# Kernel tuning notes

Hardware: AMD Instinct MI355X
Metric: run time of the kernel (lower is better)

The kernel has to match this reference:

```python
import jax, jax.numpy as jnp
import numpy as np

D_MODEL = 2048
STATE = 16
KCONV = 4
EXPAND = 2
D_INNER = D_MODEL * EXPAND
EPS = 1e-05


def setup_inputs() -> dict:
    key = jax.random.key(0)
    ks = jax.random.split(key, 10)
    s = 0.02
    x = jax.random.normal(ks[0], (2, 2048, D_MODEL), dtype=jnp.float32)
    norm_w = jnp.ones((D_MODEL,), jnp.float32)
    in_proj_w = jax.random.normal(ks[1], (D_INNER * 2, D_MODEL), jnp.float32) * s
    conv_w = jax.random.normal(ks[2], (D_INNER, 1, KCONV), jnp.float32) * s  # depthwise (O,I/g,K)
    conv_b = jnp.zeros((D_INNER,), jnp.float32)
    x_proj_w = jax.random.normal(ks[3], (STATE * 2 + 1, D_INNER), jnp.float32) * s
    dt_w = jax.random.normal(ks[4], (D_INNER, 1), jnp.float32) * s
    dt_b = jnp.zeros((D_INNER,), jnp.float32)
    A_log = jnp.log(jnp.broadcast_to(jnp.arange(1, STATE + 1, dtype=jnp.float32)[None, :], (D_INNER, STATE)))
    D_param = jnp.ones((D_INNER,), jnp.float32)
    out_proj_w = jax.random.normal(ks[5], (D_MODEL, D_INNER), jnp.float32) * s
    return {"x": x, "norm_w": norm_w, "in_proj_w": in_proj_w, "conv_w": conv_w,
            "conv_b": conv_b, "x_proj_w": x_proj_w, "dt_w": dt_w, "dt_b": dt_b,
            "A_log": A_log, "D_param": D_param, "out_proj_w": out_proj_w}


def _silu(v):
    return v * jax.nn.sigmoid(v)


def reference(x, norm_w, in_proj_w, conv_w, conv_b, x_proj_w, dt_w, dt_b, A_log, D_param, out_proj_w):
    residual = x
    # RMSNorm
    xn = x * jax.lax.rsqrt(jnp.mean(x * x, axis=-1, keepdims=True) + EPS) * norm_w
    # in_proj -> split into x_inner, z
    xz = jnp.einsum('bld,ed->ble', xn, in_proj_w)  # [B,L,2*d_inner]
    x_inner, z = jnp.split(xz, 2, axis=-1)
    # causal depthwise conv1d (torch pads K-1 both sides then truncates to L == left pad only)
    xc = jnp.transpose(x_inner, (0, 2, 1))  # [B,d_inner,L]
    xc = jax.lax.conv_general_dilated(
        xc, conv_w, window_strides=(1,), padding=[(KCONV - 1, 0)],
        dimension_numbers=('NCH', 'OIH', 'NCH'), feature_group_count=D_INNER)
    xc = xc + conv_b[None, :, None]
    xc = _silu(jnp.transpose(xc, (0, 2, 1)))  # [B,L,d_inner]
    # SSM parameter projections
    x_ssm = jnp.einsum('bld,ed->ble', xc, x_proj_w)  # [B,L,2N+1]
    dt = jax.nn.softplus(x_ssm[..., -1:] * dt_w[:, 0] + dt_b)  # [B,L,d_inner]
    B_p = x_ssm[..., :STATE]            # [B,L,N]
    C_p = x_ssm[..., STATE:2 * STATE]   # [B,L,N]
    A = -jnp.exp(A_log)                 # [d_inner,N]

    batch = x.shape[0]
    h0 = jnp.zeros((batch, D_INNER, STATE), x.dtype)

    def step(h, inp):
        dt_t, B_t, C_t, u_t = inp  # [B,d_inner],[B,N],[B,N],[B,d_inner]
        dA = jnp.exp(dt_t[..., None] * A)  # [B,d_inner,N]
        h = dA * h + (dt_t * u_t)[..., None] * B_t[:, None, :]
        y_t = jnp.sum(h * C_t[:, None, :], axis=-1) + D_param * u_t
        return h, y_t

    seq_first = lambda a: jnp.swapaxes(a, 0, 1)
    _, ys = jax.lax.scan(step, h0, (seq_first(dt), seq_first(B_p), seq_first(C_p), seq_first(xc)))
    y = jnp.swapaxes(ys, 0, 1)  # [B,L,d_inner]
    y = y * _silu(z)
    return jnp.einsum('ble,de->bld', y, out_proj_w) + residual
```

## Files before the change

### kernel.cpp

```cpp
#include <hip/hip_runtime.h>

#define NTOK   4096
#define LSEQ   2048
#define DMODEL 2048
#define DINNER 4096
#define NSTATE 16
#define NCHAIN 8192

using short8 = __attribute__((ext_vector_type(8))) short;
using f32x4  = __attribute__((ext_vector_type(4))) float;

__device__ inline float b2f(short s) {
    union { unsigned u; float f; } v;
    v.u = ((unsigned)(unsigned short)s) << 16;
    return v.f;
}
__device__ inline short f2b(float f) {
    unsigned u = __float_as_uint(f);
    unsigned r = (u + 0x7fffu + ((u >> 16) & 1u)) >> 16;
    return (short)r;
}

template <int OFF>
__device__ inline float swz(float v) {
    return __int_as_float(__builtin_amdgcn_ds_swizzle(__float_as_int(v), OFF));
}
template <int CTRL>
__device__ inline float qperm(float v) {
    return __int_as_float(
        __builtin_amdgcn_mov_dpp(__float_as_int(v), CTRL, 0xF, 0xF, true));
}

__global__ __launch_bounds__(256) void f32_to_bf16_kernel(
    const float* __restrict__ in, short* __restrict__ out, int n8) {
    int i = blockIdx.x * 256 + threadIdx.x;
    if (i >= n8) return;
    const float4* p = (const float4*)in + 2 * (size_t)i;
    float4 a = p[0], b = p[1];
    short8 s;
    s[0] = f2b(a.x); s[1] = f2b(a.y); s[2] = f2b(a.z); s[3] = f2b(a.w);
    s[4] = f2b(b.x); s[5] = f2b(b.y); s[6] = f2b(b.z); s[7] = f2b(b.w);
    *(short8*)(out + 8 * (size_t)i) = s;
}

__global__ __launch_bounds__(256) void rmsnorm_kernel(
    const float* __restrict__ x, const float* __restrict__ w,
    short* __restrict__ xn) {
    const int t = blockIdx.x, tid = threadIdx.x;
    const float4* xr = (const float4*)(x + (size_t)t * DMODEL + tid * 8);
    float4 a = xr[0], b = xr[1];
    float v[8] = {a.x, a.y, a.z, a.w, b.x, b.y, b.z, b.w};
    float ss = 0.f;
#pragma unroll
    for (int j = 0; j < 8; ++j) ss += v[j] * v[j];
#pragma unroll
    for (int o = 32; o > 0; o >>= 1) ss += __shfl_down(ss, o, 64);
    __shared__ float sred[4];
    if ((tid & 63) == 0) sred[tid >> 6] = ss;
    __syncthreads();
    float r = rsqrtf((sred[0] + sred[1] + sred[2] + sred[3]) * (1.f / DMODEL) + 1e-5f);
    const float4* wr = (const float4*)(w + tid * 8);
    float4 wa = wr[0], wb = wr[1];
    float wv[8] = {wa.x, wa.y, wa.z, wa.w, wb.x, wb.y, wb.z, wb.w};
    short8 o8;
#pragma unroll
    for (int j = 0; j < 8; ++j) o8[j] = f2b(v[j] * r * wv[j]);
    *(short8*)(xn + (size_t)t * DMODEL + tid * 8) = o8;
}

template <bool ADD_RES, bool F32OUT, bool SPLIT>
__global__ __launch_bounds__(256) void gemm_bt(
    const short* __restrict__ A, const short* __restrict__ B,
    const float* __restrict__ RES, void* __restrict__ Cp, void* __restrict__ Cp2,
    int M, int N, int K) {
    __shared__ __align__(16) short As[128 * 32];
    __shared__ __align__(16) short Bs[128 * 32];

    const int tid  = threadIdx.x;
    const int wave = tid >> 6;
    const int lane = tid & 63;
    const int lr   = lane & 15;
    const int q    = lane >> 4;
    const int m0   = blockIdx.x * 128;
    const int n0   = blockIdx.y * 128;
    const int wm   = (wave >> 1) * 64;
    const int wn   = (wave & 1) * 64;

    f32x4 acc[4][4] = {};

    for (int k0 = 0; k0 < K; k0 += 32) {
#pragma unroll
        for (int p = 0; p < 2; ++p) {
            int i16 = p * 256 + tid;
            int row = i16 >> 2, ch = i16 & 3;
            const short* ga = A + (size_t)(m0 + row) * K + k0 + ch * 8;
            const short* gb = B + (size_t)(n0 + row) * K + k0 + ch * 8;
            __builtin_amdgcn_global_load_lds(
                (const __attribute__((address_space(1))) void*)ga,
                (__attribute__((address_space(3))) void*)((char*)As + i16 * 16),
                16, 0, 0);
            __builtin_amdgcn_global_load_lds(
                (const __attribute__((address_space(1))) void*)gb,
                (__attribute__((address_space(3))) void*)((char*)Bs + i16 * 16),
                16, 0, 0);
        }
        __syncthreads();

        short8 af[4], bfr[4];
#pragma unroll
        for (int i = 0; i < 4; ++i) {
            af[i]  = *(const short8*)&As[(wm + i * 16 + lr) * 32 + q * 8];
            bfr[i] = *(const short8*)&Bs[(wn + i * 16 + lr) * 32 + q * 8];
        }
#pragma unroll
        for (int i = 0; i < 4; ++i)
#pragma unroll
            for (int j = 0; j < 4; ++j)
                acc[i][j] = __builtin_amdgcn_mfma_f32_16x16x32_bf16(
                    af[i], bfr[j], acc[i][j], 0, 0, 0);
        __syncthreads();
    }

    short* sdst = nullptr;
    int    noff = 0;
    if (SPLIT) {
        bool hi = (n0 >= DINNER);
        sdst = hi ? (short*)Cp2 : (short*)Cp;
        noff = hi ? DINNER : 0;
    }

#pragma unroll
    for (int i = 0; i < 4; ++i)
#pragma unroll
        for (int j = 0; j < 4; ++j)
#pragma unroll
            for (int r = 0; r < 4; ++r) {
                int m = m0 + wm + i * 16 + q * 4 + r;
                int n = n0 + wn + j * 16 + lr;
                float v = acc[i][j][r];
                if (SPLIT) {
                    sdst[(size_t)m * DINNER + (n - noff)] = f2b(v);
                } else {
                    size_t idx = (size_t)m * N + n;
                    if (ADD_RES) v += RES[idx];
                    if (F32OUT) ((float*)Cp)[idx] = v;
                    else        ((short*)Cp)[idx] = f2b(v);
                }
            }
}

__global__ __launch_bounds__(256) void conv_silu_t_kernel(
    const short* __restrict__ xi, const float* __restrict__ cw,
    const float* __restrict__ cb, short* __restrict__ xc,
    short* __restrict__ uT) {
    __shared__ short tin[67][72];
    __shared__ short tout[64][72];
    const int bb = blockIdx.z;
    const int l0 = blockIdx.x * 64;
    const int c0 = blockIdx.y * 64;
    const int tid = threadIdx.x;

    for (int idx = tid; idx < 67 * 8; idx += 256) {
        int row = idx >> 3, cs = (idx & 7) * 8;
        int ls = l0 - 3 + row;
        short8 v;
        if (ls >= 0) {
            v = *(const short8*)(xi + ((size_t)(bb * LSEQ + ls)) * DINNER + c0 + cs);
        } else {
#pragma unroll
            for (int j = 0; j < 8; ++j) v[j] = 0;
        }
        *(short8*)&tin[row][cs] = v;
    }
    __syncthreads();

    const int r   = tid >> 2;
    const int cb16 = (tid & 3) * 16;
    short8 a[4][2];
#pragma unroll
    for (int k = 0; k < 4; ++k) {
        a[k][0] = *(const short8*)&tin[r + k][cb16];
        a[k][1] = *(const short8*)&tin[r + k][cb16 + 8];
    }
    short o16[16];
#pragma unroll
    for (int j = 0; j < 16; ++j) {
        const int c = c0 + cb16 + j;
        float4 w4 = *(const float4*)(cw + (size_t)c * 4);
        float acc = cb[c];
        acc += b2f(a[0][j >> 3][j & 7]) * w4.x;
        acc += b2f(a[1][j >> 3][j & 7]) * w4.y;
        acc += b2f(a[2][j >> 3][j & 7]) * w4.z;
        acc += b2f(a[3][j >> 3][j & 7]) * w4.w;
        o16[j] = f2b(acc / (1.f + __expf(-acc)));
    }
    {
        short8 lo, hi;
#pragma unroll
        for (int j = 0; j < 8; ++j) { lo[j] = o16[j]; hi[j] = o16[8 + j]; }
        short* dst = xc + ((size_t)(bb * LSEQ + l0 + r)) * DINNER + c0 + cb16;
        *(short8*)dst = lo;
        *(short8*)(dst + 8) = hi;
    }
#pragma unroll
    for (int j = 0; j < 16; ++j) tout[r][cb16 + j] = o16[j];
    __syncthreads();

    const int rr = tid >> 3;
    const int l8 = (tid & 7) * 8;
#pragma unroll
    for (int p = 0; p < 2; ++p) {
        int cr = p * 32 + rr;
        short8 v;
#pragma unroll
        for (int j = 0; j < 8; ++j) v[j] = tout[l8 + j][cr];
        *(short8*)(uT + ((size_t)(bb * DINNER + c0 + cr)) * LSEQ + l0 + l8) = v;
    }
}

__global__ __launch_bounds__(256) void xproj_kernel(
    const short* __restrict__ xc, const float* __restrict__ W,
    float* __restrict__ BT, float* __restrict__ CT, float* __restrict__ s32T) {
    const int t0 = blockIdx.x * 2, tid = threadIdx.x;
    float xv0[16], xv1[16];
    {
        short8 a = *(const short8*)(xc + (size_t)t0 * DINNER + tid * 16);
        short8 b = *(const short8*)(xc + (size_t)t0 * DINNER + tid * 16 + 8);
        short8 c = *(const short8*)(xc + (size_t)(t0 + 1) * DINNER + tid * 16);
        short8 d = *(const short8*)(xc + (size_t)(t0 + 1) * DINNER + tid * 16 + 8);
#pragma unroll
        for (int j = 0; j < 8; ++j) {
            xv0[j] = b2f(a[j]); xv0[8 + j] = b2f(b[j]);
            xv1[j] = b2f(c[j]); xv1[8 + j] = b2f(d[j]);
        }
    }
    float acc0[33], acc1[33];
#pragma unroll
    for (int e = 0; e < 33; ++e) {
        const float4* wr = (const float4*)(W + (size_t)e * DINNER + tid * 16);
        float4 w0 = wr[0], w1 = wr[1], w2 = wr[2], w3 = wr[3];
        float wv[16] = {w0.x, w0.y, w0.z, w0.w, w1.x, w1.y, w1.z, w1.w,
                        w2.x, w2.y, w2.z, w2.w, w3.x, w3.y, w3.z, w3.w};
        float s0 = 0.f, s1 = 0.f;
#pragma unroll
        for (int j = 0; j < 16; ++j) { s0 += xv0[j] * wv[j]; s1 += xv1[j] * wv[j]; }
        acc0[e] = s0; acc1[e] = s1;
    }
    __shared__ float red[4][33];
#pragma unroll
    for (int tk = 0; tk < 2; ++tk) {
#pragma unroll
        for (int e = 0; e < 33; ++e) {
            float v = tk ? acc1[e] : acc0[e];
#pragma unroll
            for (int o = 32; o > 0; o >>= 1) v += __shfl_down(v, o, 64);
            if ((tid & 63) == 0) red[tid >> 6][e] = v;
        }
        __syncthreads();
        if (tid < 33) {
            float val = red[0][tid] + red[1][tid] + red[2][tid] + red[3][tid];
            const int t = t0 + tk;
            const int bb = t >> 11, l = t & (LSEQ - 1);
            if (tid < 16)
                BT[((size_t)bb * NSTATE + tid) * LSEQ + l] = val;
            else if (tid < 32)
                CT[((size_t)bb * NSTATE + (tid - 16)) * LSEQ + l] = val;
            else
                s32T[(size_t)bb * LSEQ + l] = val;
        }
        __syncthreads();
    }
}

__global__ __launch_bounds__(256) void dt_kernel(
    const float* __restrict__ s32T, const float* __restrict__ dt_w,
    const float* __restrict__ dt_b, float* __restrict__ dtT0,
    float* __restrict__ dtT1) {
    const int chain = blockIdx.x;
    const int b = chain >> 12;
    const int c = chain & (DINNER - 1);
    const float dtw = dt_w[c], dtb = dt_b[c];
    const float* src = s32T + (size_t)b * LSEQ + threadIdx.x * 8;
    float* dst = (b ? dtT1 : dtT0) + (size_t)c * LSEQ + threadIdx.x * 8;
    float4 s0 = ((const float4*)src)[0], s1 = ((const float4*)src)[1];
    float sv[8] = {s0.x, s0.y, s0.z, s0.w, s1.x, s1.y, s1.z, s1.w};
    float dv[8];
#pragma unroll
    for (int j = 0; j < 8; ++j) {
        float v = sv[j] * dtw + dtb;
        dv[j] = (v > 20.f) ? v : __logf(1.f + __expf(v));
    }
    ((float4*)dst)[0] = make_float4(dv[0], dv[1], dv[2], dv[3]);
    ((float4*)dst)[1] = make_float4(dv[4], dv[5], dv[6], dv[7]);
}

#define GQ 4
__global__ __launch_bounds__(256) void scan_state_kernel(
    const float* __restrict__ BT, const float* __restrict__ CT,
    const float* __restrict__ dtT0, const float* __restrict__ dtT1,
    const short* __restrict__ uT, const short* __restrict__ Z,
    short* __restrict__ yout,
    const float* __restrict__ A_log, const float* __restrict__ D_par) {
    const int tid   = threadIdx.x;
    const int n     = tid & 15;
    const int chain = blockIdx.x * 16 + (tid >> 4);
    const int b     = chain >> 12;
    const int c     = chain & (DINNER - 1);

    const float An = -__expf(A_log[c * NSTATE + n]);
    const float Dp = D_par[c];

    const float* Bb = BT + ((size_t)b * NSTATE + n) * LSEQ;
    const float* Cb = CT + ((size_t)b * NSTATE + n) * LSEQ;
    const float* db = (b ? dtT1 : dtT0) + (size_t)c * LSEQ;
    const short* ub = uT + (size_t)chain * LSEQ;
    const short* ue = ub + n;
    const short* zp = Z + ((size_t)b * LSEQ + n) * DINNER + c;
    short*       yp = yout + ((size_t)b * LSEQ + n) * DINNER + c;

    f32x4 Bq[GQ], Cq[GQ], dq[GQ];
    uint2 uq[GQ];
#pragma unroll
    for (int g = 0; g < GQ; ++g) {
        Bq[g] = *(const f32x4*)(Bb + g * 4);
        Cq[g] = *(const f32x4*)(Cb + g * 4);
        dq[g] = *(const f32x4*)(db + g * 4);
        uq[g] = *(const uint2*)(ub + g * 4);
    }

    float h = 0.f;
    for (int l0 = 0; l0 < LSEQ; l0 += 16) {
        const float u_n = b2f(ue[0]);
        const float z_n = b2f(zp[0]);
        float ys = 0.f;
#pragma unroll
        for (int g = 0; g < GQ; ++g) {
            f32x4 B4 = Bq[g], C4 = Cq[g], d4 = dq[g];
            uint2 u4 = uq[g];
            int lp  = l0 + 16 + g * 4;
            int lpc = (lp > LSEQ - 4) ? (LSEQ - 4) : lp;
            Bq[g] = *(const f32x4*)(Bb + lpc);
            Cq[g] = *(const f32x4*)(Cb + lpc);
            dq[g] = *(const f32x4*)(db + lpc);
            uq[g] = *(const uint2*)(ub + lpc);

            float uv[4], e[4];
#pragma unroll
            for (int i = 0; i < 4; ++i) {
                unsigned uw = (i < 2) ? u4.x : u4.y;
                union { unsigned uu; float ff; } t;
                t.uu = (i & 1) ? (uw & 0xffff0000u) : (uw << 16);
                uv[i] = t.ff;
                e[i]  = __expf(d4[i] * An);
            }
            float part[4];
#pragma unroll
            for (int i = 0; i < 4; ++i) {
                h = e[i] * h + (d4[i] * uv[i]) * B4[i];
                part[i] = h * C4[i];
            }
            float tmp[4];
#pragma unroll
            for (int i = 0; i < 4; ++i) tmp[i] = swz<0x201F>(part[i]);
#pragma unroll
            for (int i = 0; i < 4; ++i) part[i] += tmp[i];
#pragma unroll
            for (int i = 0; i < 4; ++i) tmp[i] = swz<0x101F>(part[i]);
#pragma unroll
            for (int i = 0; i < 4; ++i) part[i] += tmp[i];
#pragma unroll
            for (int i = 0; i < 4; ++i) part[i] += qperm<0x4E>(part[i]);
#pragma unroll
            for (int i = 0; i < 4; ++i) part[i] += qperm<0xB1>(part[i]);
#pragma unroll
            for (int i = 0; i < 4; ++i) ys = (n == g * 4 + i) ? part[i] : ys;
        }
        float y  = ys + Dp * u_n;
        float zg = z_n / (1.f + __expf(-z_n));
        yp[0] = f2b(y * zg);
        ue += 16;
        zp += (size_t)16 * DINNER;
        yp += (size_t)16 * DINNER;
    }
}

extern "C" void kernel_launch(void* const* d_in, const int* in_sizes, int n_in,
                              void* d_out, int out_size, void* d_ws, size_t ws_size,
                              hipStream_t stream) {
    const float* x      = (const float*)d_in[0];
    const float* norm_w = (const float*)d_in[1];
    const float* w_in   = (const float*)d_in[2];
    const float* conv_w = (const float*)d_in[3];
    const float* conv_b = (const float*)d_in[4];
    const float* w_xp   = (const float*)d_in[5];
    const float* dt_w   = (const float*)d_in[6];
    const float* dt_b   = (const float*)d_in[7];
    const float* A_log  = (const float*)d_in[8];
    const float* D_par  = (const float*)d_in[9];
    const float* w_out  = (const float*)d_in[10];
    float* out = (float*)d_out;

    char* ws = (char*)d_ws;
    short* wb   = (short*)(ws);
    short* xn   = (short*)(ws + (size_t)(32 << 20));
    short* Xi   = (short*)(ws + (size_t)(48 << 20));
    short* Zb   = (short*)(ws + (size_t)(80 << 20));
    short* xc   = (short*)(ws + (size_t)(112 << 20));
    float* BT   = (float*)(ws + (size_t)(144 << 20));
    float* CT   = (float*)(ws + (size_t)(144 << 20) + (256 << 10));
    float* s32T = (float*)(ws + (size_t)(144 << 20) + (512 << 10));
    float* dtT0 = (float*)Xi;
    float* dtT1 = out;

    f32_to_bf16_kernel<<<(2 * DINNER * DMODEL / 8) / 256, 256, 0, stream>>>(
        w_in, wb, 2 * DINNER * DMODEL / 8);
    rmsnorm_kernel<<<NTOK, 256, 0, stream>>>(x, norm_w, xn);
    gemm_bt<false, false, true><<<dim3(NTOK / 128, 8192 / 128), 256, 0, stream>>>(
        xn, wb, nullptr, Xi, Zb, NTOK, 2 * DINNER, DMODEL);
    conv_silu_t_kernel<<<dim3(LSEQ / 64, DINNER / 64, 2), 256, 0, stream>>>(
        Xi, conv_w, conv_b, xc, wb);
    xproj_kernel<<<NTOK / 2, 256, 0, stream>>>(xc, w_xp, BT, CT, s32T);
    dt_kernel<<<NCHAIN, 256, 0, stream>>>(s32T, dt_w, dt_b, dtT0, dtT1);
    scan_state_kernel<<<NCHAIN / 16, 256, 0, stream>>>(
        BT, CT, dtT0, dtT1, wb, Zb, xc, A_log, D_par);
    f32_to_bf16_kernel<<<(DMODEL * DINNER / 8) / 256, 256, 0, stream>>>(
        w_out, xn, DMODEL * DINNER / 8);
    gemm_bt<true, true, false><<<dim3(NTOK / 128, DMODEL / 128), 256, 0, stream>>>(
        xc, xn, x, out, nullptr, NTOK, DMODEL, DINNER);
}
```

Baseline: 1.080 ms.

## Process two scan chains per thread to interleave recurrences and share B/C loads

Each thread in the selective-scan kernel now advances two independent channel recurrences (A and B) that share the same batch and so reuse the same B and C loads. The grid is halved to match. The two dependent h-update chains are interleaved to hide latency, and the first ds_swizzle in the reduction becomes a DPP row-rotate-by-8. The prefetch at the tail is now skipped by a branch instead of clamping the index. This roughly doubles register use per thread and halves the number of waves, which may reduce occupancy and latency hiding.

```diff
diff --git a/kernel.cpp b/kernel.cpp
--- a/kernel.cpp
+++ b/kernel.cpp
@@ -29,6 +29,10 @@
 __device__ inline float qperm(float v) {
     return __int_as_float(
         __builtin_amdgcn_mov_dpp(__float_as_int(v), CTRL, 0xF, 0xF, true));
+}
+__device__ inline float ror8(float v) {
+    return __int_as_float(
+        __builtin_amdgcn_mov_dpp(__float_as_int(v), 0x128, 0xF, 0xF, true));
 }
 
 __global__ __launch_bounds__(256) void f32_to_bf16_kernel(
@@ -174,7 +178,7 @@
     }
     __syncthreads();
 
-    const int r   = tid >> 2;
+    const int r    = tid >> 2;
     const int cb16 = (tid & 3) * 16;
     short8 a[4][2];
 #pragma unroll
@@ -301,86 +305,117 @@
     const short* __restrict__ uT, const short* __restrict__ Z,
     short* __restrict__ yout,
     const float* __restrict__ A_log, const float* __restrict__ D_par) {
-    const int tid   = threadIdx.x;
-    const int n     = tid & 15;
-    const int chain = blockIdx.x * 16 + (tid >> 4);
-    const int b     = chain >> 12;
-    const int c     = chain & (DINNER - 1);
-
-    const float An = -__expf(A_log[c * NSTATE + n]);
-    const float Dp = D_par[c];
-
-    const float* Bb = BT + ((size_t)b * NSTATE + n) * LSEQ;
-    const float* Cb = CT + ((size_t)b * NSTATE + n) * LSEQ;
-    const float* db = (b ? dtT1 : dtT0) + (size_t)c * LSEQ;
-    const short* ub = uT + (size_t)chain * LSEQ;
-    const short* ue = ub + n;
-    const short* zp = Z + ((size_t)b * LSEQ + n) * DINNER + c;
-    short*       yp = yout + ((size_t)b * LSEQ + n) * DINNER + c;
-
-    f32x4 Bq[GQ], Cq[GQ], dq[GQ];
-    uint2 uq[GQ];
+    const int tid  = threadIdx.x;
+    const int n    = tid & 15;
+    const int slot = tid >> 4;
+    const int cA   = blockIdx.x * 32 + slot;
+    const int cB   = cA + 16;
+    const int b    = cA >> 12;
+    const int ca   = cA & (DINNER - 1);
+    const int cb2  = cB & (DINNER - 1);
+
+    const float AnA = -__expf(A_log[ca * NSTATE + n]);
+    const float AnB = -__expf(A_log[cb2 * NSTATE + n]);
+    const float DpA = D_par[ca];
+    const float DpB = D_par[cb2];
+
+    const float* Bb  = BT + ((size_t)b * NSTATE + n) * LSEQ;
+    const float* Cb  = CT + ((size_t)b * NSTATE + n) * LSEQ;
+    const float* dbA = (b ? dtT1 : dtT0) + (size_t)ca * LSEQ;
+    const float* dbB = (b ? dtT1 : dtT0) + (size_t)cb2 * LSEQ;
+    const short* ubA = uT + (size_t)cA * LSEQ;
+    const short* ubB = uT + (size_t)cB * LSEQ;
+    const short* ueA = ubA + n;
+    const short* ueB = ubB + n;
+    const short* zpA = Z + ((size_t)b * LSEQ + n) * DINNER + ca;
+    const short* zpB = Z + ((size_t)b * LSEQ + n) * DINNER + cb2;
+    short*       ypA = yout + ((size_t)b * LSEQ + n) * DINNER + ca;
+    short*       ypB = yout + ((size_t)b * LSEQ + n) * DINNER + cb2;
+
+    f32x4 Bq[GQ], Cq[GQ], dqA[GQ], dqB[GQ];
+    uint2 uqA[GQ], uqB[GQ];
 #pragma unroll
     for (int g = 0; g < GQ; ++g) {
-        Bq[g] = *(const f32x4*)(Bb + g * 4);
-        Cq[g] = *(const f32x4*)(Cb + g * 4);
-        dq[g] = *(const f32x4*)(db + g * 4);
-        uq[g] = *(const uint2*)(ub + g * 4);
-    }
-
-    float h = 0.f;
+        Bq[g]  = *(const f32x4*)(Bb + g * 4);
+        Cq[g]  = *(const f32x4*)(Cb + g * 4);
+        dqA[g] = *(const f32x4*)(dbA + g * 4);
+        dqB[g] = *(const f32x4*)(dbB + g * 4);
+        uqA[g] = *(const uint2*)(ubA + g * 4);
+        uqB[g] = *(const uint2*)(ubB + g * 4);
+    }
+
+    float hA = 0.f, hB = 0.f;
     for (int l0 = 0; l0 < LSEQ; l0 += 16) {
-        const float u_n = b2f(ue[0]);
-        const float z_n = b2f(zp[0]);
-        float ys = 0.f;
+        const float uA = b2f(ueA[0]), zA = b2f(zpA[0]);
+        const float uB = b2f(ueB[0]), zB = b2f(zpB[0]);
+        const bool refill = (l0 + 16 < LSEQ);
+        float ysA = 0.f, ysB = 0.f;
 #pragma unroll
         for (int g = 0; g < GQ; ++g) {
-            f32x4 B4 = Bq[g], C4 = Cq[g], d4 = dq[g];
-            uint2 u4 = uq[g];
-            int lp  = l0 + 16 + g * 4;
-            int lpc = (lp > LSEQ - 4) ? (LSEQ - 4) : lp;
-            Bq[g] = *(const f32x4*)(Bb + lpc);
-            Cq[g] = *(const f32x4*)(Cb + lpc);
-            dq[g] = *(const f32x4*)(db + lpc);
-            uq[g] = *(const uint2*)(ub + lpc);
-
-            float uv[4], e[4];
+            f32x4 B4 = Bq[g], C4 = Cq[g], dA4 = dqA[g], dB4 = dqB[g];
+            uint2 u4A = uqA[g], u4B = uqB[g];
+            if (refill) {
+                const int lp = l0 + 16 + g * 4;
+                Bq[g]  = *(const f32x4*)(Bb + lp);
+                Cq[g]  = *(const f32x4*)(Cb + lp);
+                dqA[g] = *(const f32x4*)(dbA + lp);
+                dqB[g] = *(const f32x4*)(dbB + lp);
+                uqA[g] = *(const uint2*)(ubA + lp);
+                uqB[g] = *(const uint2*)(ubB + lp);
+            }
+            float uvA[4], uvB[4], eA[4], eB[4];
 #pragma unroll
             for (int i = 0; i < 4; ++i) {
-                unsigned uw = (i < 2) ? u4.x : u4.y;
-                union { unsigned uu; float ff; } t;
-                t.uu = (i & 1) ? (uw & 0xffff0000u) : (uw << 16);
-                uv[i] = t.ff;
-                e[i]  = __expf(d4[i] * An);
-            }
-            float part[4];
+                unsigned wA = (i < 2) ? u4A.x : u4A.y;
+                unsigned wB = (i < 2) ? u4B.x : u4B.y;
+                union { unsigned uu; float ff; } t0, t1;
+                t0.uu = (i & 1) ? (wA & 0xffff0000u) : (wA << 16);
+                t1.uu = (i & 1) ? (wB & 0xffff0000u) : (wB << 16);
+                uvA[i] = t0.ff; uvB[i] = t1.ff;
+                eA[i] = __expf(dA4[i] * AnA);
+                eB[i] = __expf(dB4[i] * AnB);
+            }
+            float pA[4], pB[4];
 #pragma unroll
             for (int i = 0; i < 4; ++i) {
-                h = e[i] * h + (d4[i] * uv[i]) * B4[i];
-                part[i] = h * C4[i];
-            }
-            float tmp[4];
-#pragma unroll
-            for (int i = 0; i < 4; ++i) tmp[i] = swz<0x201F>(part[i]);
-#pragma unroll
-            for (int i = 0; i < 4; ++i) part[i] += tmp[i];
-#pragma unroll
-            for (int i = 0; i < 4; ++i) tmp[i] = swz<0x101F>(part[i]);
-#pragma unroll
-            for (int i = 0; i < 4; ++i) part[i] += tmp[i];
-#pragma unroll
-            for (int i = 0; i < 4; ++i) part[i] += qperm<0x4E>(part[i]);
-#pragma unroll
-            for (int i = 0; i < 4; ++i) part[i] += qperm<0xB1>(part[i]);
-#pragma unroll
-            for (int i = 0; i < 4; ++i) ys = (n == g * 4 + i) ? part[i] : ys;
-        }
-        float y  = ys + Dp * u_n;
-        float zg = z_n / (1.f + __expf(-z_n));
-        yp[0] = f2b(y * zg);
-        ue += 16;
-        zp += (size_t)16 * DINNER;
-        yp += (size_t)16 * DINNER;
+                hA = eA[i] * hA + (dA4[i] * uvA[i]) * B4[i];
+                pA[i] = hA * C4[i];
+            }
+#pragma unroll
+            for (int i = 0; i < 4; ++i) {
+                hB = eB[i] * hB + (dB4[i] * uvB[i]) * B4[i];
+                pB[i] = hB * C4[i];
+            }
+            float tA[4], tB[4];
+#pragma unroll
+            for (int i = 0; i < 4; ++i) { tA[i] = ror8(pA[i]); tB[i] = ror8(pB[i]); }
+#pragma unroll
+            for (int i = 0; i < 4; ++i) { pA[i] += tA[i]; pB[i] += tB[i]; }
+#pragma unroll
+            for (int i = 0; i < 4; ++i) { tA[i] = swz<0x101F>(pA[i]); tB[i] = swz<0x101F>(pB[i]); }
+#pragma unroll
+            for (int i = 0; i < 4; ++i) { pA[i] += tA[i]; pB[i] += tB[i]; }
+#pragma unroll
+            for (int i = 0; i < 4; ++i) { pA[i] += qperm<0x4E>(pA[i]); pB[i] += qperm<0x4E>(pB[i]); }
+#pragma unroll
+            for (int i = 0; i < 4; ++i) { pA[i] += qperm<0xB1>(pA[i]); pB[i] += qperm<0xB1>(pB[i]); }
+#pragma unroll
+            for (int i = 0; i < 4; ++i) {
+                ysA = (n == g * 4 + i) ? pA[i] : ysA;
+                ysB = (n == g * 4 + i) ? pB[i] : ysB;
+            }
+        }
+        {
+            float yA  = ysA + DpA * uA;
+            float zgA = zA / (1.f + __expf(-zA));
+            ypA[0] = f2b(yA * zgA);
+            float yB  = ysB + DpB * uB;
+            float zgB = zB / (1.f + __expf(-zB));
+            ypB[0] = f2b(yB * zgB);
+        }
+        ueA += 16; ueB += 16;
+        zpA += (size_t)16 * DINNER; zpB += (size_t)16 * DINNER;
+        ypA += (size_t)16 * DINNER; ypB += (size_t)16 * DINNER;
     }
 }
 
@@ -421,7 +456,7 @@
         Xi, conv_w, conv_b, xc, wb);
     xproj_kernel<<<NTOK / 2, 256, 0, stream>>>(xc, w_xp, BT, CT, s32T);
     dt_kernel<<<NCHAIN, 256, 0, stream>>>(s32T, dt_w, dt_b, dtT0, dtT1);
-    scan_state_kernel<<<NCHAIN / 16, 256, 0, stream>>>(
+    scan_state_kernel<<<NCHAIN / 32, 256, 0, stream>>>(
         BT, CT, dtT0, dtT1, wb, Zb, xc, A_log, D_par);
     f32_to_bf16_kernel<<<(DMODEL * DINNER / 8) / 256, 256, 0, stream>>>(
         w_out, xn, DMODEL * DINNER / 8);
```

Result: faster. 1.016 ms (-5.9%).
